# Performance work log

Hardware: AMD Instinct MI355X
Metric: run time of the kernel (lower is better)

Reference implementation:

```python
import jax, jax.numpy as jnp
import numpy as np

B, S, HID = 2, 2048, 2048
H, KV, D = 32, 8, 64
GROUPS = H // KV
THETA = 10000.0
SCALE = D ** -0.5
NEG = -1e9


def setup_inputs() -> dict:
    key = jax.random.key(0)
    ks = jax.random.split(key, 5)
    x = jax.random.normal(ks[0], (B, S, 2 * HID), dtype=jnp.float32)
    # Linear weights stored as [in, out] (torch stores [out, in]; y = x @ W.T there)
    Wq = jax.random.normal(ks[1], (2 * HID, H * D), dtype=jnp.float32) * 0.02
    Wk = jax.random.normal(ks[2], (2 * HID, KV * D), dtype=jnp.float32) * 0.02
    Wv = jax.random.normal(ks[3], (2 * HID, KV * D), dtype=jnp.float32) * 0.02
    Wo = jax.random.normal(ks[4], (H * D, HID), dtype=jnp.float32) * 0.02
    # additive causal mask, broadcastable to [B, 1, S, S]
    causal = jnp.tril(jnp.ones((S, S), dtype=bool))
    attention_mask = jnp.where(causal, 0.0, NEG)[None, None].astype(jnp.float32)
    position_ids = jnp.broadcast_to(jnp.arange(S, dtype=jnp.int32)[None, :], (B, S))
    return {"combined_states": x, "attention_mask": attention_mask,
            "position_ids": position_ids, "Wq": Wq, "Wk": Wk, "Wv": Wv, "Wo": Wo}


def _rotate_half(x):
    x1, x2 = jnp.split(x, 2, axis=-1)
    return jnp.concatenate([-x2, x1], axis=-1)


def _rope_cos_sin(position_ids, dtype):
    inv_freq = 1.0 / (THETA ** (jnp.arange(0, D, 2, dtype=jnp.float32) / D))  # [D/2]
    freqs = position_ids.astype(jnp.float32)[..., None] * inv_freq  # [B, S, D/2]
    emb = jnp.concatenate([freqs, freqs], axis=-1)  # [B, S, D]
    return jnp.cos(emb).astype(dtype), jnp.sin(emb).astype(dtype)


def reference(combined_states, attention_mask, position_ids, Wq, Wk, Wv, Wo):
    x = combined_states
    q = (x @ Wq).reshape(B, S, H, D).transpose(0, 2, 1, 3)    # [B, H, S, D]
    k = (x @ Wk).reshape(B, S, KV, D).transpose(0, 2, 1, 3)   # [B, KV, S, D]
    v = (x @ Wv).reshape(B, S, KV, D).transpose(0, 2, 1, 3)
    cos, sin = _rope_cos_sin(position_ids, x.dtype)           # [B, S, D]
    cos, sin = cos[:, None], sin[:, None]                     # [B, 1, S, D]
    q = q * cos + _rotate_half(q) * sin
    k = k * cos + _rotate_half(k) * sin
    k = jnp.repeat(k, GROUPS, axis=1)                         # [B, H, S, D]
    v = jnp.repeat(v, GROUPS, axis=1)
    scores = jnp.einsum('bhqd,bhkd->bhqk', q, k) * SCALE + attention_mask
    probs = jax.nn.softmax(scores.astype(jnp.float32), axis=-1).astype(q.dtype)
    attn = jnp.einsum('bhqk,bhkd->bhqd', probs, v)            # [B, H, S, D]
    attn = attn.transpose(0, 2, 1, 3).reshape(B, S, H * D)
    return attn @ Wo
```

## Files before the change

kernel.cpp:

```cpp
#include <hip/hip_runtime.h>

#define S_LEN 2048
#define BATCH 2
#define HEADS 32
#define KVH   8
#define DH    64

typedef unsigned short u16;
typedef unsigned int   u32;
typedef u16   u16x8 __attribute__((ext_vector_type(8)));
typedef u16   u16x4 __attribute__((ext_vector_type(4)));
typedef short s16x8 __attribute__((ext_vector_type(8)));
typedef float f32x4 __attribute__((ext_vector_type(4)));
typedef u32   u32x2 __attribute__((ext_vector_type(2)));

__device__ __forceinline__ u16 f2bf(float f) {
    unsigned x; __builtin_memcpy(&x, &f, 4);
    x += 0x7fffu + ((x >> 16) & 1u);
    return (u16)(x >> 16);
}
__device__ __forceinline__ float bf2f(u16 u) {
    unsigned x = ((unsigned)u) << 16; float f; __builtin_memcpy(&f, &x, 4); return f;
}
__device__ __forceinline__ float fexp2(float x) {
#if __has_builtin(__builtin_amdgcn_exp2f)
    return __builtin_amdgcn_exp2f(x);
#else
    return exp2f(x);
#endif
}
__device__ __forceinline__ void gll16(const void* g, void* l) {
    __builtin_amdgcn_global_load_lds((const __attribute__((address_space(1))) unsigned*)g,
                                     (__attribute__((address_space(3))) unsigned*)l, 16, 0, 0);
}

__global__ __launch_bounds__(256) void k_f32_to_bf16(const float* __restrict__ src,
                                                     u16* __restrict__ dst, int n4) {
    int i = blockIdx.x * 256 + threadIdx.x;
    if (i < n4) {
        f32x4 v = ((const f32x4*)src)[i];
        u16x4 o;
        o.x = f2bf(v.x); o.y = f2bf(v.y); o.z = f2bf(v.z); o.w = f2bf(v.w);
        ((u16x4*)dst)[i] = o;
    }
}

__global__ __launch_bounds__(256) void k_wprep(const float* __restrict__ Wq, const float* __restrict__ Wk,
                                               const float* __restrict__ Wv, const float* __restrict__ Wo,
                                               u16* __restrict__ wqkvt, u16* __restrict__ wot) {
    __shared__ float t[32][33];
    int id = blockIdx.x;
    const float* src; u16* dst; int srcCols, dstStride, dstRowOff, bx, by;
    if (id < 8192)       { src = Wq; dst = wqkvt; srcCols = 2048; dstStride = 4096; dstRowOff = 0;    bx = id & 127; by = id >> 7; }
    else if (id < 10240) { id -= 8192;  src = Wk; dst = wqkvt; srcCols = 512; dstStride = 4096; dstRowOff = 2048; bx = id & 127; by = id >> 7; }
    else if (id < 12288) { id -= 10240; src = Wv; dst = wqkvt; srcCols = 512; dstStride = 4096; dstRowOff = 2560; bx = id & 127; by = id >> 7; }
    else                 { id -= 12288; src = Wo; dst = wot;   srcCols = 2048; dstStride = 2048; dstRowOff = 0;   bx = id & 63;  by = id >> 6; }
    int r0 = bx * 32, c0 = by * 32;
    int tx = threadIdx.x & 31, ty = threadIdx.x >> 5;
#pragma unroll
    for (int i = 0; i < 4; ++i)
        t[ty + 8 * i][tx] = src[(size_t)(r0 + ty + 8 * i) * srcCols + (c0 + tx)];
    __syncthreads();
#pragma unroll
    for (int i = 0; i < 4; ++i)
        dst[(size_t)(dstRowOff + c0 + ty + 8 * i) * dstStride + (r0 + tx)] = f2bf(t[tx][ty + 8 * i]);
}

template <int OUT_BF16>
__global__ __launch_bounds__(256) void k_gemm_bt(const u16* __restrict__ A,
                                                 const u16* __restrict__ Bt,
                                                 void* __restrict__ Cout,
                                                 int M, int N, int K) {
    __shared__ __align__(16) u16 As[8192];
    __shared__ __align__(16) u16 Bs[8192];
    int tid = threadIdx.x;
    int wave = tid >> 6, lane = tid & 63, m15 = lane & 15, quad = lane >> 4;
    int wm = (wave >> 1) * 64, wn = (wave & 1) * 64;
    int m0 = blockIdx.y * 128, n0 = blockIdx.x * 128;

    f32x4 acc[4][4];
#pragma unroll
    for (int i = 0; i < 4; ++i)
#pragma unroll
        for (int j = 0; j < 4; ++j) acc[i][j] = (f32x4){0.f, 0.f, 0.f, 0.f};

    int rl8 = lane >> 3;
    int sg8 = ((lane & 7) ^ rl8) * 8;
    const u16* Ag = A  + (size_t)(m0 + wave * 32 + rl8) * K + sg8;
    const u16* Bg = Bt + (size_t)(n0 + wave * 32 + rl8) * K + sg8;
    u16* Asl = As + (wave * 32) * 64;
    u16* Bsl = Bs + (wave * 32) * 64;
    int swq = m15 & 7;

    for (int k0 = 0; k0 < K; k0 += 64) {
        __syncthreads();
#pragma unroll
        for (int i = 0; i < 4; ++i) {
            gll16(Ag + (size_t)(8 * i) * K, Asl + (8 * i) * 64);
            gll16(Bg + (size_t)(8 * i) * K, Bsl + (8 * i) * 64);
        }
        Ag += 64; Bg += 64;
        __syncthreads();

#pragma unroll
        for (int kk = 0; kk < 2; ++kk) {
            int sgr = ((kk * 4 + quad) ^ swq) * 8;
            s16x8 af[4], bfr[4];
#pragma unroll
            for (int mt = 0; mt < 4; ++mt)
                af[mt] = *(const s16x8*)&As[(wm + mt * 16 + m15) * 64 + sgr];
#pragma unroll
            for (int nt = 0; nt < 4; ++nt)
                bfr[nt] = *(const s16x8*)&Bs[(wn + nt * 16 + m15) * 64 + sgr];
#pragma unroll
            for (int mt = 0; mt < 4; ++mt)
#pragma unroll
                for (int nt = 0; nt < 4; ++nt)
                    acc[mt][nt] = __builtin_amdgcn_mfma_f32_16x16x32_bf16(af[mt], bfr[nt], acc[mt][nt], 0, 0, 0);
        }
    }

#pragma unroll
    for (int mt = 0; mt < 4; ++mt)
#pragma unroll
        for (int nt = 0; nt < 4; ++nt)
#pragma unroll
            for (int r = 0; r < 4; ++r) {
                size_t row = m0 + wm + mt * 16 + quad * 4 + r;
                size_t col = n0 + wn + nt * 16 + m15;
                float v = acc[mt][nt][r];
                if (OUT_BF16) ((u16*)Cout)[row * N + col] = f2bf(v);
                else          ((float*)Cout)[row * N + col] = v;
            }
}

__global__ __launch_bounds__(256) void k_vtrans(const u16* __restrict__ qkv, u16* __restrict__ vt) {
    __shared__ u16 t[64][72];
    int s0 = blockIdx.x * 64;
    int bkv = blockIdx.y;
    int tid = threadIdx.x;
    int row = tid >> 2, seg = tid & 3;
    int b = bkv >> 3, kv = bkv & 7;
    const u16* src = qkv + (size_t)(b * S_LEN + s0 + row) * 3072 + 2560 + kv * 64 + seg * 16;
    *(u16x8*)&t[row][seg * 16]     = *(const u16x8*)(src);
    *(u16x8*)&t[row][seg * 16 + 8] = *(const u16x8*)(src + 8);
    __syncthreads();
    int d = tid >> 2, sseg = tid & 3;
    u16x8 o0, o1;
#pragma unroll
    for (int j = 0; j < 8; ++j) {
        o0[j] = t[(j & 3) * 16 + sseg * 4 + (j >> 2)][d];
        o1[j] = t[(j & 3) * 16 + sseg * 4 + (j >> 2) + 2][d];
    }
    u16* dst = vt + ((size_t)bkv * 64 + d) * S_LEN + s0 + sseg * 16;
    *(u16x8*)(dst)     = o0;
    *(u16x8*)(dst + 8) = o1;
}

__global__ __launch_bounds__(256) void k_rope(const u16* __restrict__ qkv,
                                              const int* __restrict__ pos_ids,
                                              u16* __restrict__ qo, u16* __restrict__ ko) {
    int bs = blockIdx.x;
    int b = bs >> 11, s = bs & 2047;
    int tid = threadIdx.x;
    float pos = (float)pos_ids[bs];
    const u16* row = qkv + (size_t)bs * 3072;

#pragma unroll
    for (int p = tid; p < 1024; p += 256) {
        int h = p >> 5, i = p & 31;
        float inv = fexp2((float)i * -0.4152410119f);
        float ang = pos * inv;
        float sn, c; __sincosf(ang, &sn, &c);
        float a = bf2f(row[h * 64 + i]);
        float bq = bf2f(row[h * 64 + i + 32]);
        size_t base = ((size_t)(b * HEADS + h) * S_LEN + s) * DH;
        qo[base + i]      = f2bf(a * c - bq * sn);
        qo[base + i + 32] = f2bf(bq * c + a * sn);
    }
    {
        int p = tid;
        if (p < 256) {
            int kv = p >> 5, i = p & 31;
            float inv = fexp2((float)i * -0.4152410119f);
            float ang = pos * inv;
            float sn, c; __sincosf(ang, &sn, &c);
            float a = bf2f(row[2048 + kv * 64 + i]);
            float bk = bf2f(row[2048 + kv * 64 + i + 32]);
            size_t base = ((size_t)(b * KVH + kv) * S_LEN + s) * DH;
            ko[base + i]      = f2bf(a * c - bk * sn);
            ko[base + i + 32] = f2bf(bk * c + a * sn);
        }
    }
}

__global__ __launch_bounds__(256) void k_attn(const u16* __restrict__ q, const u16* __restrict__ k,
                                              const u16* __restrict__ vt, u16* __restrict__ out) {
    __shared__ __align__(16) u16 Qs[4096];
    __shared__ __align__(16) u16 Ks[8192];
    __shared__ __align__(16) u16 Vts[8192];
    __shared__ __align__(16) u16 Ps[4 * 16 * 72];
    int bh = blockIdx.y;
    int b = bh >> 5, h = bh & 31, kvh = h >> 2;
    int tid = threadIdx.x, wave = tid >> 6, lane = tid & 63, m15 = lane & 15, quad = lane >> 4;

    const u16* qhb = q + (size_t)(b * HEADS + h) * S_LEN * DH;
    const u16* kb  = k + (size_t)(b * KVH + kvh) * S_LEN * DH;
    const u16* vb  = vt + (size_t)(b * KVH + kvh) * DH * S_LEN;
    u16* PsW = &Ps[wave * 16 * 72];
    const float C = 0.1803368801f;

    int rl8 = lane >> 3;
    int sg8 = ((lane & 7) ^ rl8) * 8;
    int swq = m15 & 7;
    int vrow = lane >> 4;
    int vgrp = lane & 15;

    for (int half = 0; half < 2; ++half) {
        int jt = half ? (31 - (int)blockIdx.x) : (int)blockIdx.x;
        int q0 = jt * 64;
        __syncthreads();
        {
            const u16* qg = qhb + (size_t)(q0 + wave * 16 + rl8) * DH + sg8;
            gll16(qg,          Qs + (wave * 16) * 64);
            gll16(qg + 8 * DH, Qs + (wave * 16 + 8) * 64);
        }

        float lsum[4];
        f32x4 oacc[4];
#pragma unroll
        for (int r = 0; r < 4; ++r) lsum[r] = 0.f;
#pragma unroll
        for (int dt = 0; dt < 4; ++dt) oacc[dt] = (f32x4){0.f, 0.f, 0.f, 0.f};

        for (int ib = 0; ib <= jt; ib += 2) {
            int kk0 = ib * 64;
            int nsub = (jt - ib >= 1) ? 2 : 1;
            __syncthreads();
            {
                const u16* kg = kb + (size_t)(kk0 + wave * 32 + rl8) * DH + sg8;
#pragma unroll
                for (int i = 0; i < 4; ++i)
                    gll16(kg + (size_t)(8 * i) * DH, Ks + (wave * 32 + 8 * i) * 64);
#pragma unroll
                for (int i = 0; i < 4; ++i) {
                    int d = wave * 16 + 4 * i + vrow;
                    const u16* vg = vb + (size_t)d * S_LEN + kk0 + ((vgrp ^ (d & 7)) * 8);
                    gll16(vg, Vts + (wave * 16 + 4 * i) * 128);
                }
            }
            __syncthreads();

            for (int sub = 0; sub < nsub; ++sub) {
                f32x4 sacc[4];
#pragma unroll
                for (int nt = 0; nt < 4; ++nt) sacc[nt] = (f32x4){0.f, 0.f, 0.f, 0.f};
#pragma unroll
                for (int kk = 0; kk < 2; ++kk) {
                    int sgr = ((kk * 4 + quad) ^ swq) * 8;
                    s16x8 aF = *(const s16x8*)&Qs[(wave * 16 + m15) * 64 + sgr];
#pragma unroll
                    for (int nt = 0; nt < 4; ++nt) {
                        s16x8 bF = *(const s16x8*)&Ks[(sub * 64 + nt * 16 + m15) * 64 + sgr];
                        sacc[nt] = __builtin_amdgcn_mfma_f32_16x16x32_bf16(aF, bF, sacc[nt], 0, 0, 0);
                    }
                }

                bool dsub = (kk0 + sub * 64) == q0;
#pragma unroll
                for (int r = 0; r < 4; ++r) {
                    int qrr = wave * 16 + quad * 4 + r;
                    float p0[4];
#pragma unroll
                    for (int nt = 0; nt < 4; ++nt) {
                        float s2 = sacc[nt][r] * C - 12.0f;
                        if (dsub && (nt * 16 + m15 > qrr)) s2 = -1e30f;
                        p0[nt] = fexp2(s2);
                        lsum[r] += p0[nt];
                    }
                    unsigned a0, a1, a2, a3;
                    __builtin_memcpy(&a0, &p0[0], 4); __builtin_memcpy(&a1, &p0[1], 4);
                    __builtin_memcpy(&a2, &p0[2], 4); __builtin_memcpy(&a3, &p0[3], 4);
                    u32x2 w;
                    w.x = (a0 >> 16) | (a1 & 0xffff0000u);
                    w.y = (a2 >> 16) | (a3 & 0xffff0000u);
                    *(u32x2*)&PsW[(quad * 4 + r) * 72 + m15 * 4] = w;
                }

#pragma unroll
                for (int kk = 0; kk < 2; ++kk) {
                    s16x8 aF = *(const s16x8*)&PsW[m15 * 72 + kk * 32 + quad * 8];
                    int g = (sub * 8 + kk * 4 + quad) ^ swq;
#pragma unroll
                    for (int dt = 0; dt < 4; ++dt) {
                        s16x8 bF = *(const s16x8*)&Vts[(dt * 16 + m15) * 128 + g * 8];
                        oacc[dt] = __builtin_amdgcn_mfma_f32_16x16x32_bf16(aF, bF, oacc[dt], 0, 0, 0);
                    }
                }
            }
        }

#pragma unroll
        for (int r = 0; r < 4; ++r) {
            float ls = lsum[r];
#pragma unroll
            for (int off = 1; off < 16; off <<= 1) ls += __shfl_xor(ls, off, 64);
            float inv = 1.f / ls;
            int qrow = q0 + wave * 16 + quad * 4 + r;
#pragma unroll
            for (int dt = 0; dt < 4; ++dt)
                out[((size_t)(b * S_LEN) + qrow) * (size_t)(HEADS * DH) + h * DH + dt * 16 + m15] =
                    f2bf(oacc[dt][r] * inv);
        }
    }
}

extern "C" void kernel_launch(void* const* d_in, const int* in_sizes, int n_in,
                              void* d_out, int out_size, void* d_ws, size_t ws_size,
                              hipStream_t stream) {
    const float* x  = (const float*)d_in[0];
    const int*   pos = (const int*)d_in[2];
    const float* Wq = (const float*)d_in[3];
    const float* Wk = (const float*)d_in[4];
    const float* Wv = (const float*)d_in[5];
    const float* Wo = (const float*)d_in[6];

    char* ws = (char*)d_ws;
    const size_t NEED = 92274688;
    if (ws_size < NEED) return;

    u16* xbf   = (u16*)(ws);
    u16* vt    = (u16*)(ws + 16777216);
    u16* wqkvt = (u16*)(ws + 33554432);
    u16* wot   = (u16*)(ws + 58720256);
    u16* qkv   = (u16*)(ws + 67108864);
    u16* qro   = wqkvt;
    u16* kro   = qro + 8388608;
    u16* attn  = xbf;

    k_f32_to_bf16<<<16384, 256, 0, stream>>>(x, xbf, 4194304);
    k_wprep<<<16384, 256, 0, stream>>>(Wq, Wk, Wv, Wo, wqkvt, wot);
    { dim3 g(24, 32); k_gemm_bt<1><<<g, 256, 0, stream>>>(xbf, wqkvt, qkv, 4096, 3072, 4096); }
    { dim3 g(32, 16); k_vtrans<<<g, 256, 0, stream>>>(qkv, vt); }
    k_rope<<<4096, 256, 0, stream>>>(qkv, pos, qro, kro);
    { dim3 g(16, 64); k_attn<<<g, 256, 0, stream>>>(qro, kro, vt, attn); }
    { dim3 g(16, 32); k_gemm_bt<0><<<g, 256, 0, stream>>>(attn, wot, (float*)d_out, 4096, 2048, 2048); }
}
```

Baseline: 435.1 us.

## Replace QKV projection GEMM with 256x256 8-wave multi-stage pipelined kernel

Adds a new bf16 GEMM kernel with 256x256 output tiles, 8 waves per block, and an 8-slot LDS ring filled by direct global-to-LDS loads. Explicit barriers, waitcnts and setprio interleave the loads with MFMA work. It is used for the QKV projection in place of the 128x128 kernel, to raise data reuse and hide memory latency. The cost is higher register and LDS pressure, 128 KB of LDS per block, and only 192 blocks, which risks leaving compute units underused on a 256-CU part.

```diff
diff --git a/kernel.cpp b/kernel.cpp
--- a/kernel.cpp
+++ b/kernel.cpp
@@ -132,6 +132,172 @@
                 if (OUT_BF16) ((u16*)Cout)[row * N + col] = f2bf(v);
                 else          ((float*)Cout)[row * N + col] = v;
             }
+}
+
+__global__ __launch_bounds__(512, 2) void k_gemm8p(const u16* __restrict__ A,
+                                                   const u16* __restrict__ Bt,
+                                                   u16* __restrict__ Cout,
+                                                   int M, int N, int K) {
+    __shared__ __align__(16) u16 Ls[8][8192];
+    const int tid = threadIdx.x;
+    const int wave = tid >> 6, lane = tid & 63;
+    const int m15 = lane & 15, quad = lane >> 4;
+    const int wm = wave >> 2, wn = wave & 3;
+    const int rl8 = lane >> 3;
+    const int sg8 = ((lane & 7) ^ rl8) * 8;
+    const int m0 = blockIdx.y * 256, n0 = blockIdx.x * 256;
+
+    const u16* Abase = A  + (size_t)(m0 + wave * 16 + rl8) * K + sg8;
+    const u16* Bbase = Bt + (size_t)(n0 + wave * 16 + rl8) * K + sg8;
+    u16* Lst = &Ls[0][0] + wave * 1024;
+    const int aro = (wm * 16 + m15) * 64;
+    const int bro = (wn * 16 + m15) * 64;
+    const int sx = m15 & 7;
+
+    f32x4 acc[8][4];
+#pragma unroll
+    for (int i = 0; i < 8; ++i)
+#pragma unroll
+        for (int j = 0; j < 4; ++j) acc[i][j] = (f32x4){0.f, 0.f, 0.f, 0.f};
+    s16x8 rA0[8], rA1[8], rB0[4], rB1[4];
+
+#define STG8(slot, c, t) do { \
+    const u16* gsrc_ = ((c) & 1) ? Abase : Bbase; \
+    size_t off_ = (size_t)(((c) >> 1) * 128) * K + (size_t)(t) * 64; \
+    u16* ld_ = Lst + (slot) * 8192; \
+    gll16(gsrc_ + off_, ld_); \
+    gll16(gsrc_ + off_ + (size_t)8 * K, ld_ + 512); \
+} while (0)
+
+#define RDA8(slot, rg) do { \
+    const u16* sb_ = &Ls[slot][0] + aro; \
+    _Pragma("unroll") \
+    for (int mt_ = 0; mt_ < 4; ++mt_) \
+        _Pragma("unroll") \
+        for (int kk_ = 0; kk_ < 2; ++kk_) \
+            rg[mt_ * 2 + kk_] = *(const s16x8*)&sb_[mt_ * 2048 + (((kk_ * 4 + quad) ^ sx) * 8)]; \
+} while (0)
+
+#define RDB8(slot, rg) do { \
+    const u16* sb_ = &Ls[slot][0] + bro; \
+    _Pragma("unroll") \
+    for (int nt_ = 0; nt_ < 2; ++nt_) \
+        _Pragma("unroll") \
+        for (int kk_ = 0; kk_ < 2; ++kk_) \
+            rg[nt_ * 2 + kk_] = *(const s16x8*)&sb_[nt_ * 4096 + (((kk_ * 4 + quad) ^ sx) * 8)]; \
+} while (0)
+
+#define MM8(ra, rb, mi, ni) do { \
+    _Pragma("unroll") \
+    for (int mt_ = 0; mt_ < 4; ++mt_) \
+        _Pragma("unroll") \
+        for (int nt_ = 0; nt_ < 2; ++nt_) \
+            _Pragma("unroll") \
+            for (int kk_ = 0; kk_ < 2; ++kk_) \
+                acc[(mi) + mt_][(ni) + nt_] = __builtin_amdgcn_mfma_f32_16x16x32_bf16( \
+                    ra[mt_ * 2 + kk_], rb[nt_ * 2 + kk_], acc[(mi) + mt_][(ni) + nt_], 0, 0, 0); \
+} while (0)
+
+#define BAR8() asm volatile("s_barrier" ::: "memory")
+#define LGKM8() do { asm volatile("s_waitcnt lgkmcnt(0)" ::: "memory"); \
+                     __builtin_amdgcn_sched_barrier(0); } while (0)
+#define GUARD8(more) do { \
+    if (more) asm volatile("s_waitcnt vmcnt(6)" ::: "memory"); \
+    else      asm volatile("s_waitcnt vmcnt(0)" ::: "memory"); \
+} while (0)
+
+    const int NT2 = K >> 7;
+
+    STG8(0, 0, 0); STG8(1, 1, 0); STG8(2, 2, 0); STG8(3, 3, 0);
+    STG8(4, 0, 1); STG8(5, 1, 1); STG8(6, 2, 1);
+    asm volatile("s_waitcnt vmcnt(6)" ::: "memory");
+    BAR8();
+
+    for (int it = 0; it < NT2; ++it) {
+        const int t2 = 2 * it + 2, t3 = 2 * it + 3;
+        const bool more = (it < NT2 - 1);
+
+        RDB8(0, rB0);
+        STG8(7, 3, 2 * it + 1);
+        BAR8(); LGKM8();
+        if (it) {
+            __builtin_amdgcn_s_setprio(1);
+            MM8(rA1, rB1, 4, 2);
+            __builtin_amdgcn_s_setprio(0);
+        }
+        BAR8();
+        RDA8(1, rA0);
+        if (more) STG8(0, 0, t2);
+        BAR8(); LGKM8();
+        __builtin_amdgcn_s_setprio(1);
+        MM8(rA0, rB0, 0, 0);
+        __builtin_amdgcn_s_setprio(0);
+        BAR8();
+        RDB8(2, rB1);
+        if (more) STG8(1, 1, t2);
+        BAR8(); LGKM8();
+        __builtin_amdgcn_s_setprio(1);
+        MM8(rA0, rB1, 0, 2);
+        __builtin_amdgcn_s_setprio(0);
+        BAR8();
+        RDA8(3, rA1);
+        if (more) STG8(2, 2, t2);
+        BAR8(); LGKM8();
+        __builtin_amdgcn_s_setprio(1);
+        MM8(rA1, rB0, 4, 0);
+        __builtin_amdgcn_s_setprio(0);
+        GUARD8(more);
+        BAR8();
+        RDB8(4, rB0);
+        if (more) STG8(3, 3, t2);
+        BAR8(); LGKM8();
+        __builtin_amdgcn_s_setprio(1);
+        MM8(rA1, rB1, 4, 2);
+        __builtin_amdgcn_s_setprio(0);
+        BAR8();
+        RDA8(5, rA0);
+        if (more) STG8(4, 0, t3);
+        BAR8(); LGKM8();
+        __builtin_amdgcn_s_setprio(1);
+        MM8(rA0, rB0, 0, 0);
+        __builtin_amdgcn_s_setprio(0);
+        BAR8();
+        RDB8(6, rB1);
+        if (more) STG8(5, 1, t3);
+        BAR8(); LGKM8();
+        __builtin_amdgcn_s_setprio(1);
+        MM8(rA0, rB1, 0, 2);
+        __builtin_amdgcn_s_setprio(0);
+        BAR8();
+        RDA8(7, rA1);
+        if (more) STG8(6, 2, t3);
+        BAR8(); LGKM8();
+        __builtin_amdgcn_s_setprio(1);
+        MM8(rA1, rB0, 4, 0);
+        __builtin_amdgcn_s_setprio(0);
+        GUARD8(more);
+        BAR8();
+    }
+    MM8(rA1, rB1, 4, 2);
+
+#pragma unroll
+    for (int i = 0; i < 8; ++i) {
+        size_t row = (size_t)(m0 + (i & 3) * 32 + wm * 16 + (i >> 2) * 128 + quad * 4);
+#pragma unroll
+        for (int j = 0; j < 4; ++j) {
+            size_t col = (size_t)(n0 + (j & 1) * 64 + wn * 16 + (j >> 1) * 128 + m15);
+#pragma unroll
+            for (int r = 0; r < 4; ++r)
+                Cout[(row + r) * N + col] = f2bf(acc[i][j][r]);
+        }
+    }
+#undef STG8
+#undef RDA8
+#undef RDB8
+#undef MM8
+#undef BAR8
+#undef LGKM8
+#undef GUARD8
 }
 
 __global__ __launch_bounds__(256) void k_vtrans(const u16* __restrict__ qkv, u16* __restrict__ vt) {
@@ -340,7 +506,7 @@
 
     k_f32_to_bf16<<<16384, 256, 0, stream>>>(x, xbf, 4194304);
     k_wprep<<<16384, 256, 0, stream>>>(Wq, Wk, Wv, Wo, wqkvt, wot);
-    { dim3 g(24, 32); k_gemm_bt<1><<<g, 256, 0, stream>>>(xbf, wqkvt, qkv, 4096, 3072, 4096); }
+    { dim3 g(12, 16); k_gemm8p<<<g, 512, 0, stream>>>(xbf, wqkvt, qkv, 4096, 3072, 4096); }
     { dim3 g(32, 16); k_vtrans<<<g, 256, 0, stream>>>(qkv, vt); }
     k_rope<<<4096, 256, 0, stream>>>(qkv, pos, qro, kro);
     { dim3 g(16, 64); k_attn<<<g, 256, 0, stream>>>(qro, kro, vt, attn); }
```

Result: faster. 407.7 us (-6.3%).
